# Optimization experiments

Hardware: AMD Instinct MI355X
Metric: run time of the kernel (lower is better)

The kernel has to match this reference:

```python
import jax, jax.numpy as jnp
import numpy as np

D_MODEL = 1024
N_HEADS = 16


def setup_inputs() -> dict:
    key = jax.random.key(0)
    ks = jax.random.split(key, 5)
    B, L, D = 2, 2048, D_MODEL
    x = jax.random.normal(ks[0], (B, L, D), dtype=jnp.float32)
    # Linear params (torch nn.Linear: y = x @ W.T + b); store as (in, out) for einsum.
    s_attn = 1.0 / np.sqrt(D)
    W_attn = jax.random.uniform(ks[1], (D, 3 * D), jnp.float32, -s_attn, s_attn)
    b_attn = jax.random.uniform(ks[2], (3 * D,), jnp.float32, -s_attn, s_attn)
    W_proj = jax.random.uniform(ks[3], (D, D), jnp.float32, -s_attn, s_attn)
    b_proj = jax.random.uniform(ks[4], (D,), jnp.float32, -s_attn, s_attn)
    return {"x": x, "W_attn": W_attn, "b_attn": b_attn, "W_proj": W_proj, "b_proj": b_proj}


def reference(x, W_attn, b_attn, W_proj, b_proj):
    B, L, D = x.shape
    H = N_HEADS
    hd = D // H
    qkv = jnp.einsum('bld,de->ble', x, W_attn) + b_attn  # [B,L,3D]
    # Faithful to source bug: q and v are both taken from the k projection.
    k_lin = qkv[:, :, D:2 * D]
    k = k_lin.reshape(B, L, H, hd).transpose(0, 2, 1, 3)  # [B,H,L,hd]
    q = k
    v = k
    att = jnp.einsum('bhqd,bhkd->bhqk', q, k) / jnp.sqrt(jnp.float32(hd))
    att = jax.nn.softmax(att, axis=3)
    out = jnp.einsum('bhqk,bhkd->bhqd', att, v)  # [B,H,L,hd]
    out = out.transpose(0, 2, 1, 3).reshape(B, L, D)
    return jnp.einsum('bld,de->ble', out, W_proj) + b_proj
```

## Files before the change

### kernel.cpp

```cpp
#include <hip/hip_runtime.h>
#include <hip/hip_bf16.h>

typedef __attribute__((ext_vector_type(8))) short short8;
typedef __attribute__((ext_vector_type(4))) float f32x4;
typedef __attribute__((ext_vector_type(16))) float f32x16;
typedef unsigned short u16;
typedef unsigned int u32;

static __device__ __forceinline__ u16 f2b(float f) {
  __hip_bfloat16 h = __float2bfloat16(f);
  return __builtin_bit_cast(u16, h);
}
static __device__ __forceinline__ float b2f(u16 v) {
  return __builtin_bit_cast(float, ((u32)v) << 16);
}
static __device__ __forceinline__ u32 pk2(float lo, float hi) {
  return (u32)f2b(lo) | ((u32)f2b(hi) << 16);
}
static __device__ __forceinline__ u32 cvtpk(float lo, float hi) {
  u32 r;
  asm("v_cvt_pk_bf16_f32 %0, %1, %2" : "=v"(r) : "v"(lo), "v"(hi));
  return r;
}

static __device__ __forceinline__ void gload16(const void* g, void* l) {
  __builtin_amdgcn_global_load_lds((const __attribute__((address_space(1))) void*)g,
                                   (__attribute__((address_space(3))) void*)l, 16, 0, 0);
}

static __device__ __forceinline__ void barrier_fenced() {
  __builtin_amdgcn_sched_barrier(0);
  asm volatile("" ::: "memory");
  __builtin_amdgcn_s_barrier();
  __builtin_amdgcn_sched_barrier(0);
  asm volatile("" ::: "memory");
}

__global__ __launch_bounds__(256) void prep(const float4* __restrict__ x4,
                                            uint2* __restrict__ xb,
                                            const float* __restrict__ W_attn,
                                            u16* __restrict__ Wkt,
                                            const float* __restrict__ W_proj,
                                            u16* __restrict__ Wpt) {
  __shared__ u16 tile[32][33];
  int bid = blockIdx.x, t = threadIdx.x;
  if (bid < 4096) {
    int i = bid * 256 + t;
    float4 v = x4[i];
    uint2 o;
    o.x = pk2(v.x, v.y);
    o.y = pk2(v.z, v.w);
    xb[i] = o;
    return;
  }
  const float* in;
  u16* out;
  int in_rs, col_off, blk;
  if (bid < 5120) {
    in = W_attn; out = Wkt; in_rs = 3072; col_off = 1024; blk = bid - 4096;
  } else {
    in = W_proj; out = Wpt; in_rs = 1024; col_off = 0; blk = bid - 5120;
  }
  int tx = t & 31, ty = t >> 5;
  int r0 = (blk >> 5) * 32, c0 = (blk & 31) * 32;
#pragma unroll
  for (int i = 0; i < 4; ++i) {
    int r = r0 + ty + i * 8;
    tile[ty + i * 8][tx] = f2b(in[(size_t)r * in_rs + col_off + c0 + tx]);
  }
  __syncthreads();
#pragma unroll
  for (int i = 0; i < 4; ++i) {
    int c = c0 + ty + i * 8;
    out[(size_t)c * 1024 + r0 + tx] = tile[tx][ty + i * 8];
  }
}

template <int MODE>
__global__ __launch_bounds__(256) void gemm_bias(const u16* __restrict__ A,
                                                 const u16* __restrict__ Bt,
                                                 const float* __restrict__ bias,
                                                 void* __restrict__ Cp, u16* __restrict__ Ktp,
                                                 int M, int N, int K) {
  __shared__ char lds[3][24576];
  int tid = threadIdx.x, lane = tid & 63, wid = tid >> 6;
  int lr = lane & 15, lh = lane >> 4;
  int p = blockIdx.x;
  int m0 = (p >> 3) << 6, n0 = (p & 7) << 7;
  int wm = wid >> 1, wn = wid & 1;
  f32x4 acc[2][4] = {};
  int srow = lane >> 3;
  int scol = ((lane & 7) << 4) ^ (srow << 4);
  const char* Ab = (const char*)A;
  const char* Bb = (const char*)Bt;
  int r0 = wid * 8;
  const int NT = K >> 6;

  auto stage = [&](char* buf, int k0) {
    char* lA = buf;
    char* lB = buf + 8192;
    gload16(Ab + ((size_t)(m0 + r0 + srow) * K + k0) * 2 + scol, lA + r0 * 128);
    gload16(Ab + ((size_t)(m0 + 32 + r0 + srow) * K + k0) * 2 + scol, lA + (32 + r0) * 128);
#pragma unroll
    for (int i = 0; i < 4; ++i)
      gload16(Bb + ((size_t)(n0 + i * 32 + r0 + srow) * K + k0) * 2 + scol,
              lB + (i * 32 + r0) * 128);
  };

  stage(lds[0], 0);
  stage(lds[1], 64);
  for (int t = 0; t < NT; ++t) {
    if (t + 1 < NT)
      asm volatile("s_waitcnt vmcnt(6) lgkmcnt(0)" ::: "memory");
    else
      asm volatile("s_waitcnt vmcnt(0) lgkmcnt(0)" ::: "memory");
    barrier_fenced();
    char* lA = lds[t % 3];
    char* lB = lA + 8192;
    short8 af[2][2], bfr[4][2];
#pragma unroll
    for (int mi = 0; mi < 2; ++mi)
#pragma unroll
      for (int ks = 0; ks < 2; ++ks) {
        int row = wm * 32 + mi * 16 + lr;
        af[mi][ks] = *(const short8*)(lA + row * 128 + ((ks * 64 + lh * 16) ^ ((row & 7) << 4)));
      }
#pragma unroll
    for (int ni = 0; ni < 4; ++ni)
#pragma unroll
      for (int ks = 0; ks < 2; ++ks) {
        int row = wn * 64 + ni * 16 + lr;
        bfr[ni][ks] = *(const short8*)(lB + row * 128 + ((ks * 64 + lh * 16) ^ ((row & 7) << 4)));
      }
    __builtin_amdgcn_s_setprio(1);
#pragma unroll
    for (int ks = 0; ks < 2; ++ks)
#pragma unroll
      for (int mi = 0; mi < 2; ++mi)
#pragma unroll
        for (int ni = 0; ni < 4; ++ni)
          acc[mi][ni] = __builtin_amdgcn_mfma_f32_16x16x32_bf16(af[mi][ks], bfr[ni][ks],
                                                                acc[mi][ni], 0, 0, 0);
    __builtin_amdgcn_s_setprio(0);
    if (t + 2 < NT) stage(lds[(t + 2) % 3], (t + 2) << 6);
  }
#pragma unroll
  for (int mi = 0; mi < 2; ++mi)
#pragma unroll
    for (int ni = 0; ni < 4; ++ni) {
      int col = n0 + wn * 64 + ni * 16 + lr;
      float bz = bias[col];
      int row0 = m0 + wm * 32 + mi * 16 + lh * 4;
      if (MODE == 1) {
#pragma unroll
        for (int r = 0; r < 4; ++r)
          ((float*)Cp)[(size_t)(row0 + r) * N + col] = acc[mi][ni][r] + bz;
      } else {
        ushort4 q;
        u16* qa = (u16*)&q;
#pragma unroll
        for (int r = 0; r < 4; ++r) {
          u16 v = f2b(acc[mi][ni][r] + bz);
          qa[r] = v;
          ((u16*)Cp)[(size_t)(row0 + r) * N + col] = v;
        }
        *(ushort4*)(Ktp + ((size_t)((row0 >> 11) * 1024 + col)) * 2048 + (row0 & 2047)) = q;
      }
    }
}

__global__ __launch_bounds__(128) void flash_attn(const u16* __restrict__ Kb,
                                                  const u16* __restrict__ Kt,
                                                  u16* __restrict__ AO) {
  __shared__ char kv[2][16384];
  const float S2 = 0.125f * 1.44269504088896340736f;
  int tid = threadIdx.x, lane = tid & 63, wid = tid >> 6;
  int ql = lane & 31, half = lane >> 5;
  int rb = blockIdx.x;
  int bid = (rb & 7) * 128 + (rb >> 3);
  int qt = bid & 31, h = (bid >> 5) & 15, b = bid >> 9;
  int qbase = b * 2048 + qt * 64 + wid * 32;
  int hc = h * 64;
  short8 qfr[4];
#pragma unroll
  for (int ds = 0; ds < 4; ++ds) {
    short8 raw = *(const short8*)(Kb + (size_t)(qbase + ql) * 1024 + hc + ds * 16 + half * 8);
    short8 q;
#pragma unroll
    for (int j = 0; j < 8; ++j) q[j] = (short)f2b(b2f((u16)raw[j]) * S2);
    qfr[ds] = q;
  }
  const short8 ones = {0x3F80, 0x3F80, 0x3F80, 0x3F80, 0x3F80, 0x3F80, 0x3F80, 0x3F80};
  f32x16 acc0 = {}, acc1 = {}, accs = {};
  int srow = lane >> 3;
  int scol = ((lane & 7) << 4) ^ (srow << 4);
  const char* Kbase = (const char*)Kb + (size_t)(b * 2048) * 2048 + hc * 2;
  const char* Vbase = (const char*)Kt + (size_t)((b * 16 + h) * 64) * 4096;

  auto stage = [&](char* buf, int kt) {
    const char* kp = Kbase + (size_t)(kt * 64) * 2048;
    const char* vp = Vbase + (size_t)(kt * 128);
    char* lk = buf;
    char* lv = buf + 8192;
#pragma unroll
    for (int j = 0; j < 4; ++j) {
      int grp = j * 2 + wid;
      int row = grp * 8 + srow;
      gload16(kp + (size_t)row * 2048 + scol, lk + grp * 8 * 128);
      gload16(vp + (size_t)row * 4096 + scol, lv + grp * 8 * 128);
    }
  };

  stage(kv[0], 0);
  for (int kt = 0; kt < 32; ++kt) {
    asm volatile("s_waitcnt vmcnt(0) lgkmcnt(0)" ::: "memory");
    barrier_fenced();
    if (kt + 1 < 32) stage(kv[(kt + 1) & 1], kt + 1);
    const char* lk = kv[kt & 1];
    const char* lv = lk + 8192;
    short8 kf[2][4];
#pragma unroll
    for (int kb = 0; kb < 2; ++kb)
#pragma unroll
      for (int ds = 0; ds < 4; ++ds) {
        int row = kb * 32 + ql;
        kf[kb][ds] = *(const short8*)(lk + row * 128 + ((ds * 32 + half * 16) ^ ((row & 7) << 4)));
      }
    f32x16 s0 = {}, s1 = {};
    __builtin_amdgcn_s_setprio(1);
#pragma unroll
    for (int ds = 0; ds < 4; ++ds) {
      s0 = __builtin_amdgcn_mfma_f32_32x32x16_bf16(kf[0][ds], qfr[ds], s0, 0, 0, 0);
      s1 = __builtin_amdgcn_mfma_f32_32x32x16_bf16(kf[1][ds], qfr[ds], s1, 0, 0, 0);
    }
    __builtin_amdgcn_s_setprio(0);
    short8 vf0[4], vf1[4];
#pragma unroll
    for (int ks = 0; ks < 4; ++ks) {
      int row0 = ql, row1 = 32 + ql;
      vf0[ks] = *(const short8*)(lv + row0 * 128 + ((ks * 32 + half * 16) ^ ((row0 & 7) << 4)));
      vf1[ks] = *(const short8*)(lv + row1 * 128 + ((ks * 32 + half * 16) ^ ((row1 & 7) << 4)));
    }
    float p[32];
#pragma unroll
    for (int i = 0; i < 16; ++i) p[i] = __builtin_amdgcn_exp2f(s0[i]);
#pragma unroll
    for (int i = 0; i < 16; ++i) p[16 + i] = __builtin_amdgcn_exp2f(s1[i]);
    u32 w0[8], w1[8];
#pragma unroll
    for (int g = 0; g < 8; ++g) {
      int idx = (g >> 2) * 16 + (g & 3) * 4;
      w0[g] = cvtpk(p[idx], p[idx + 1]);
      w1[g] = cvtpk(p[idx + 2], p[idx + 3]);
    }
    short8 pa[4];
#pragma unroll
    for (int ks = 0; ks < 4; ++ks) {
      u32 a0 = w0[2 * ks], b0 = w0[2 * ks + 1];
      u32 a1 = w1[2 * ks], b1 = w1[2 * ks + 1];
      asm volatile("v_permlane32_swap_b32 %0, %1" : "+v"(a0), "+v"(b0));
      asm volatile("v_permlane32_swap_b32 %0, %1" : "+v"(a1), "+v"(b1));
      uint4 words = {a0, a1, b0, b1};
      pa[ks] = __builtin_bit_cast(short8, words);
    }
    __builtin_amdgcn_s_setprio(1);
#pragma unroll
    for (int ks = 0; ks < 4; ++ks) {
      acc0 = __builtin_amdgcn_mfma_f32_32x32x16_bf16(pa[ks], vf0[ks], acc0, 0, 0, 0);
      acc1 = __builtin_amdgcn_mfma_f32_32x32x16_bf16(pa[ks], vf1[ks], acc1, 0, 0, 0);
      accs = __builtin_amdgcn_mfma_f32_32x32x16_bf16(pa[ks], ones, accs, 0, 0, 0);
    }
    __builtin_amdgcn_s_setprio(0);
  }
#pragma unroll
  for (int reg = 0; reg < 16; ++reg) {
    int ridx = (reg & 3) + 8 * (reg >> 2) + 4 * half;
    float iv = __builtin_amdgcn_rcpf(accs[reg]);
    int grow = qbase + ridx;
    AO[(size_t)grow * 1024 + hc + ql] = f2b(acc0[reg] * iv);
    AO[(size_t)grow * 1024 + hc + 32 + ql] = f2b(acc1[reg] * iv);
  }
}


extern "C" void kernel_launch(void* const* d_in, const int* in_sizes, int n_in, void* d_out,
                              int out_size, void* d_ws, size_t ws_size, hipStream_t stream) {
  const float* x = (const float*)d_in[0];
  const float* W_attn = (const float*)d_in[1];
  const float* b_attn = (const float*)d_in[2];
  const float* W_proj = (const float*)d_in[3];
  const float* b_proj = (const float*)d_in[4];
  float* out = (float*)d_out;
  char* ws = (char*)d_ws;
  u16* xb = (u16*)(ws);
  u16* Kb = (u16*)(ws + 8388608);
  u16* Kt = (u16*)(ws + 16777216);
  u16* Wkt = (u16*)(ws + 25165824);
  u16* Wpt = (u16*)(ws + 27262976);

  prep<<<6144, 256, 0, stream>>>((const float4*)x, (uint2*)xb, W_attn, Wkt, W_proj, Wpt);
  gemm_bias<0><<<512, 256, 0, stream>>>(xb, Wkt, b_attn + 1024, (void*)Kb, Kt, 4096, 1024, 1024);
  u16* AO = xb;
  flash_attn<<<1024, 128, 0, stream>>>(Kb, Kt, AO);
  gemm_bias<1><<<512, 256, 0, stream>>>(AO, Wpt, b_proj, (void*)out, nullptr, 4096, 1024, 1024);
}
```

Baseline: 100.6 us.

## Split attention KV range in two and merge partials with bf16 atomics

Each attention block now covers 128 query rows with four waves, and each query tile is handled by two blocks that each process half of the key range. The unnormalised outputs are added into a zeroed buffer with packed bf16 atomic adds, and the row sums go into a float buffer with float atomics. A new norm_o kernel then divides by the row sums before the output projection. The aim is more concurrent waves and a shorter serial KV loop per block. In exchange it adds two memsets and an extra kernel launch, and summing partials in bf16 loses precision.

Measured after the change: 116.6 us. 1.16x slower.

```diff
diff --git a/kernel.cpp b/kernel.cpp
--- a/kernel.cpp
+++ b/kernel.cpp
@@ -21,6 +21,9 @@
   u32 r;
   asm("v_cvt_pk_bf16_f32 %0, %1, %2" : "=v"(r) : "v"(lo), "v"(hi));
   return r;
+}
+static __device__ __forceinline__ void atomPk(u16* p, u32 d) {
+  asm volatile("global_atomic_pk_add_bf16 %0, %1, off" ::"v"(p), "v"(d) : "memory");
 }
 
 static __device__ __forceinline__ void gload16(const void* g, void* l) {
@@ -169,17 +172,18 @@
     }
 }
 
-__global__ __launch_bounds__(128) void flash_attn(const u16* __restrict__ Kb,
+__global__ __launch_bounds__(256) void flash_attn(const u16* __restrict__ Kb,
                                                   const u16* __restrict__ Kt,
-                                                  u16* __restrict__ AO) {
+                                                  u16* __restrict__ Oacc,
+                                                  float* __restrict__ Ssum) {
   __shared__ char kv[2][16384];
   const float S2 = 0.125f * 1.44269504088896340736f;
   int tid = threadIdx.x, lane = tid & 63, wid = tid >> 6;
   int ql = lane & 31, half = lane >> 5;
   int rb = blockIdx.x;
   int bid = (rb & 7) * 128 + (rb >> 3);
-  int qt = bid & 31, h = (bid >> 5) & 15, b = bid >> 9;
-  int qbase = b * 2048 + qt * 64 + wid * 32;
+  int kvh = bid & 1, qt = (bid >> 1) & 15, h = (bid >> 5) & 15, b = bid >> 9;
+  int qbase = b * 2048 + qt * 128 + wid * 32;
   int hc = h * 64;
   short8 qfr[4];
 #pragma unroll
@@ -203,20 +207,20 @@
     char* lk = buf;
     char* lv = buf + 8192;
 #pragma unroll
-    for (int j = 0; j < 4; ++j) {
-      int grp = j * 2 + wid;
-      int row = grp * 8 + srow;
-      gload16(kp + (size_t)row * 2048 + scol, lk + grp * 8 * 128);
-      gload16(vp + (size_t)row * 4096 + scol, lv + grp * 8 * 128);
+    for (int j = 0; j < 2; ++j) {
+      int row = wid * 8 + j * 32 + srow;
+      gload16(kp + (size_t)row * 2048 + scol, lk + (wid * 8 + j * 32) * 128);
+      gload16(vp + (size_t)row * 4096 + scol, lv + (wid * 8 + j * 32) * 128);
     }
   };
 
-  stage(kv[0], 0);
-  for (int kt = 0; kt < 32; ++kt) {
+  int kt0 = kvh * 16;
+  stage(kv[0], kt0);
+  for (int i = 0; i < 16; ++i) {
     asm volatile("s_waitcnt vmcnt(0) lgkmcnt(0)" ::: "memory");
     barrier_fenced();
-    if (kt + 1 < 32) stage(kv[(kt + 1) & 1], kt + 1);
-    const char* lk = kv[kt & 1];
+    if (i + 1 < 16) stage(kv[(i + 1) & 1], kt0 + i + 1);
+    const char* lk = kv[i & 1];
     const char* lv = lk + 8192;
     short8 kf[2][4];
 #pragma unroll
@@ -243,9 +247,9 @@
     }
     float p[32];
 #pragma unroll
-    for (int i = 0; i < 16; ++i) p[i] = __builtin_amdgcn_exp2f(s0[i]);
-#pragma unroll
-    for (int i = 0; i < 16; ++i) p[16 + i] = __builtin_amdgcn_exp2f(s1[i]);
+    for (int j = 0; j < 16; ++j) p[j] = __builtin_amdgcn_exp2f(s0[j]);
+#pragma unroll
+    for (int j = 0; j < 16; ++j) p[16 + j] = __builtin_amdgcn_exp2f(s1[j]);
     u32 w0[8], w1[8];
 #pragma unroll
     for (int g = 0; g < 8; ++g) {
@@ -275,11 +279,33 @@
 #pragma unroll
   for (int reg = 0; reg < 16; ++reg) {
     int ridx = (reg & 3) + 8 * (reg >> 2) + 4 * half;
-    float iv = __builtin_amdgcn_rcpf(accs[reg]);
     int grow = qbase + ridx;
-    AO[(size_t)grow * 1024 + hc + ql] = f2b(acc0[reg] * iv);
-    AO[(size_t)grow * 1024 + hc + 32 + ql] = f2b(acc1[reg] * iv);
-  }
+    float o0 = acc0[reg], o1 = acc1[reg];
+    float o0n = __shfl_xor(o0, 1);
+    float o1n = __shfl_xor(o1, 1);
+    if ((ql & 1) == 0) {
+      atomPk(Oacc + (size_t)grow * 1024 + hc + ql, cvtpk(o0, o0n));
+      atomPk(Oacc + (size_t)grow * 1024 + hc + 32 + ql, cvtpk(o1, o1n));
+    }
+    if (ql == 0) atomicAdd(&Ssum[grow * 16 + h], accs[reg]);
+  }
+}
+
+__global__ __launch_bounds__(256) void norm_o(uint4* __restrict__ O4,
+                                              const float* __restrict__ S) {
+  int i = blockIdx.x * 256 + threadIdx.x;
+  uint4 w = O4[i];
+  int row = i >> 7;
+  int h = (i & 127) >> 3;
+  float inv = __builtin_amdgcn_rcpf(S[row * 16 + h]);
+  u32* wp = (u32*)&w;
+#pragma unroll
+  for (int j = 0; j < 4; ++j) {
+    float lo = b2f((u16)(wp[j] & 0xFFFF)) * inv;
+    float hi = b2f((u16)(wp[j] >> 16)) * inv;
+    wp[j] = cvtpk(lo, hi);
+  }
+  O4[i] = w;
 }
 
 
@@ -300,7 +326,9 @@
 
   prep<<<6144, 256, 0, stream>>>((const float4*)x, (uint2*)xb, W_attn, Wkt, W_proj, Wpt);
   gemm_bias<0><<<512, 256, 0, stream>>>(xb, Wkt, b_attn + 1024, (void*)Kb, Kt, 4096, 1024, 1024);
-  u16* AO = xb;
-  flash_attn<<<1024, 128, 0, stream>>>(Kb, Kt, AO);
-  gemm_bias<1><<<512, 256, 0, stream>>>(AO, Wpt, b_proj, (void*)out, nullptr, 4096, 1024, 1024);
-}
+  hipMemsetAsync(xb, 0, 8388608, stream);
+  hipMemsetAsync(Wkt, 0, 262144, stream);
+  flash_attn<<<1024, 256, 0, stream>>>(Kb, Kt, xb, (float*)Wkt);
+  norm_o<<<2048, 256, 0, stream>>>((uint4*)xb, (const float*)Wkt);
+  gemm_bias<1><<<512, 256, 0, stream>>>(xb, Wpt, b_proj, (void*)out, nullptr, 4096, 1024, 1024);
+}
```
